# Performance work log

Measured on AMD Instinct MI355X. Metric: run time of the kernel, lower is better.

## Reference

```python
import jax, jax.numpy as jnp
import numpy as np

N_NODES = 50000
N_EDGES = 400000
NODE_F = 128
EDGE_F = 64
HID = 128
N_LAYERS = 2


def _mlp(x, w1, b1, w2, b2):
    # Linear -> ReLU -> Linear
    return jnp.maximum(x @ w1 + b1, 0.0) @ w2 + b2


def setup_inputs() -> dict:
    key = jax.random.key(0)
    ks = jax.random.split(key, 24)
    s = 0.02
    inp = {
        "node_features": jax.random.normal(ks[0], (N_NODES, NODE_F), jnp.float32),
        "edge_list": jax.random.randint(ks[1], (N_EDGES, 2), 0, N_NODES, jnp.int32),
        "edge_features": jax.random.normal(ks[2], (N_EDGES, EDGE_F), jnp.float32),
        "num_nodes": N_NODES,
        # node encoder
        "ne_w1": jax.random.normal(ks[3], (NODE_F, HID), jnp.float32) * s,
        "ne_b1": jnp.zeros((HID,), jnp.float32),
        "ne_w2": jax.random.normal(ks[4], (HID, HID), jnp.float32) * s,
        "ne_b2": jnp.zeros((HID,), jnp.float32),
        # edge encoder
        "ee_w1": jax.random.normal(ks[5], (EDGE_F, HID), jnp.float32) * s,
        "ee_b1": jnp.zeros((HID,), jnp.float32),
        "ee_w2": jax.random.normal(ks[6], (HID, HID), jnp.float32) * s,
        "ee_b2": jnp.zeros((HID,), jnp.float32),
        # message layers (stacked over num_layers)
        "ml_w1": jax.random.normal(ks[7], (N_LAYERS, 3 * HID, HID), jnp.float32) * s,
        "ml_b1": jnp.zeros((N_LAYERS, HID), jnp.float32),
        "ml_w2": jax.random.normal(ks[8], (N_LAYERS, HID, HID), jnp.float32) * s,
        "ml_b2": jnp.zeros((N_LAYERS, HID), jnp.float32),
        # aggregation
        "agg_w1": jax.random.normal(ks[9], (HID, HID), jnp.float32) * s,
        "agg_b1": jnp.zeros((HID,), jnp.float32),
        "agg_w2": jax.random.normal(ks[10], (HID, HID), jnp.float32) * s,
        "agg_b2": jnp.zeros((HID,), jnp.float32),
    }
    return inp


def reference(node_features, edge_list, edge_features, num_nodes,
              ne_w1, ne_b1, ne_w2, ne_b2,
              ee_w1, ee_b1, ee_w2, ee_b2,
              ml_w1, ml_b1, ml_w2, ml_b2,
              agg_w1, agg_b1, agg_w2, agg_b2):
    node_emb = _mlp(node_features, ne_w1, ne_b1, ne_w2, ne_b2)   # [N, H]
    edge_emb = _mlp(edge_features, ee_w1, ee_b1, ee_w2, ee_b2)   # [E, H]
    src = edge_list[:, 0]
    dst = edge_list[:, 1]
    for l in range(ml_w1.shape[0]):
        h_s = node_emb[src]                                      # [E, H] gather
        h_d = node_emb[dst]                                      # [E, H] gather
        # message src->dst and dst->src (the torch loop does both directions)
        m_fwd = _mlp(jnp.concatenate([h_s, edge_emb, h_d], axis=-1),
                     ml_w1[l], ml_b1[l], ml_w2[l], ml_b2[l])     # [E, H]
        m_bwd = _mlp(jnp.concatenate([h_d, edge_emb, h_s], axis=-1),
                     ml_w1[l], ml_b1[l], ml_w2[l], ml_b2[l])     # [E, H]
        new_node_emb = node_emb.at[dst].add(m_fwd).at[src].add(m_bwd)
        node_emb = _mlp(new_node_emb, agg_w1, agg_b1, agg_w2, agg_b2)
    return node_emb
```

## Files before the change

### kernel.cpp

```cpp
#include <hip/hip_runtime.h>

typedef float fx4 __attribute__((ext_vector_type(4)));
typedef float f32x4 __attribute__((ext_vector_type(4)));
typedef unsigned short us4v __attribute__((ext_vector_type(4)));
typedef unsigned short us8 __attribute__((ext_vector_type(8)));
typedef __bf16 bf8 __attribute__((ext_vector_type(8)));

static __device__ __forceinline__ fx4 ld4(const float* p) {
    return *reinterpret_cast<const fx4*>(p);
}
static __device__ __forceinline__ void st4(float* p, fx4 v) {
    *reinterpret_cast<fx4*>(p) = v;
}
static __device__ __forceinline__ unsigned short f2bf(float f) {
    union { float f; unsigned int i; } x; x.f = f;
    unsigned int r = x.i + 0x7FFF + ((x.i >> 16) & 1);
    return (unsigned short)(r >> 16);
}
static __device__ __forceinline__ float bf2f(unsigned int u) {
    union { unsigned int i; float f; } x; x.i = u << 16; return x.f;
}
static __device__ __forceinline__ us4v pk4(f32x4 v) {
    us4v u;
    #pragma unroll
    for (int j = 0; j < 4; ++j) u[j] = f2bf(v[j]);
    return u;
}

static __device__ __forceinline__ f32x4 mfma16(us8 a, us8 b, f32x4 c) {
    return __builtin_amdgcn_mfma_f32_16x16x32_bf16(
        __builtin_bit_cast(bf8, a), __builtin_bit_cast(bf8, b), c, 0, 0, 0);
}

template <int K1, bool AF32>
static __device__ __forceinline__ void loadA(
    const void* __restrict__ Av, int row0, int ar, int ak, int kk, int M, us8 a[2])
{
    #pragma unroll
    for (int m = 0; m < 2; ++m) {
        int row = row0 + m * 16 + ar;
        us8 t = 0;
        if (row < M) {
            if (AF32) {
                const float* ap = (const float*)Av + (size_t)row * K1 + kk * 32 + ak;
                fx4 x0 = ld4(ap), x1 = ld4(ap + 4);
                #pragma unroll
                for (int j = 0; j < 4; ++j) { t[j] = f2bf(x0[j]); t[4 + j] = f2bf(x1[j]); }
            } else {
                t = *reinterpret_cast<const us8*>(
                    (const unsigned short*)Av + (size_t)row * K1 + kk * 32 + ak);
            }
        }
        a[m] = t;
    }
}

template <int K1, bool AF32, bool BIAS, bool RELU, bool OUTF, bool OUTB, bool XMODE>
__global__ __launch_bounds__(256) void mfma_gemm(
    const void* __restrict__ Av, const unsigned short* __restrict__ Wt,
    const float* __restrict__ bias,
    float* __restrict__ outF, unsigned short* __restrict__ outB,
    const float* __restrict__ resid, const int* __restrict__ startp,
    int M, int ntiles)
{
    constexpr int KP = K1 + 8;
    __shared__ unsigned short Ws[128 * KP];
    const int tid = threadIdx.x;
    const int lane = tid & 63;
    const int wv = tid >> 6;

    constexpr int C8 = K1 / 8;
    for (int i = tid; i < 128 * C8; i += 256) {
        int r = i / C8, c = (i % C8) * 8;
        *reinterpret_cast<us8*>(&Ws[r * KP + c]) =
            *reinterpret_cast<const us8*>(&Wt[r * K1 + c]);
    }
    __syncthreads();

    const int ar = lane & 15;
    const int ak = (lane >> 4) * 8;
    const int q = lane >> 4;

    for (int tile = blockIdx.x; tile < ntiles; tile += gridDim.x) {
        const int row0 = tile * 128 + wv * 32;

        f32x4 acc[2][8];
        #pragma unroll
        for (int m = 0; m < 2; ++m)
            #pragma unroll
            for (int nt = 0; nt < 8; ++nt) acc[m][nt] = {0.f, 0.f, 0.f, 0.f};

        #pragma unroll
        for (int kk = 0; kk < K1 / 32; ++kk) {
            us8 a[2];
            loadA<K1, AF32>(Av, row0, ar, ak, kk, M, a);
            #pragma unroll
            for (int nt = 0; nt < 8; ++nt) {
                us8 b = *reinterpret_cast<const us8*>(&Ws[(nt * 16 + ar) * KP + kk * 32 + ak]);
                acc[0][nt] = mfma16(b, a[0], acc[0][nt]);
                acc[1][nt] = mfma16(b, a[1], acc[1][nt]);
            }
        }

        #pragma unroll
        for (int m = 0; m < 2; ++m) {
            int r = row0 + m * 16 + (lane & 15);
            if (r >= M) continue;
            float deg = 0.f;
            if (XMODE) deg = (float)(startp[r + 1] - startp[r]);
            #pragma unroll
            for (int nt = 0; nt < 8; ++nt) {
                int c0 = nt * 16 + q * 4;
                f32x4 o = acc[m][nt];
                if (XMODE) {
                    fx4 bb = ld4(bias + c0);
                    fx4 rr = ld4(resid + (size_t)r * 128 + c0);
                    #pragma unroll
                    for (int j = 0; j < 4; ++j) o[j] += rr[j] + deg * bb[j];
                } else if (BIAS) {
                    fx4 bb = ld4(bias + c0);
                    #pragma unroll
                    for (int j = 0; j < 4; ++j) o[j] += bb[j];
                }
                if (RELU) {
                    #pragma unroll
                    for (int j = 0; j < 4; ++j) o[j] = fmaxf(o[j], 0.f);
                }
                if (OUTF) st4(outF + (size_t)r * 128 + c0, o);
                if (OUTB) *reinterpret_cast<us4v*>(&outB[(size_t)r * 128 + c0]) = pk4(o);
            }
        }
    }
}

__global__ __launch_bounds__(256) void mfma_gemm_dual(
    const float* __restrict__ A, const unsigned short* __restrict__ Wt,
    unsigned short* __restrict__ out1, unsigned short* __restrict__ out2,
    int M, int ntiles)
{
    constexpr int KP = 136;
    __shared__ unsigned short Ws[256 * KP];
    const int tid = threadIdx.x;
    const int lane = tid & 63;
    const int wv = tid >> 6;

    for (int i = tid; i < 256 * 16; i += 256) {
        int r = i >> 4, c = (i & 15) * 8;
        *reinterpret_cast<us8*>(&Ws[r * KP + c]) =
            *reinterpret_cast<const us8*>(&Wt[r * 128 + c]);
    }
    __syncthreads();

    const int ar = lane & 15;
    const int ak = (lane >> 4) * 8;
    const int q = lane >> 4;

    for (int tile = blockIdx.x; tile < ntiles; tile += gridDim.x) {
        const int row0 = tile * 128 + wv * 32;

        f32x4 acc[2][16];
        #pragma unroll
        for (int m = 0; m < 2; ++m)
            #pragma unroll
            for (int nt = 0; nt < 16; ++nt) acc[m][nt] = {0.f, 0.f, 0.f, 0.f};

        #pragma unroll
        for (int kk = 0; kk < 4; ++kk) {
            us8 a[2];
            loadA<128, true>(A, row0, ar, ak, kk, M, a);
            #pragma unroll
            for (int nt = 0; nt < 16; ++nt) {
                us8 b = *reinterpret_cast<const us8*>(&Ws[(nt * 16 + ar) * KP + kk * 32 + ak]);
                acc[0][nt] = mfma16(b, a[0], acc[0][nt]);
                acc[1][nt] = mfma16(b, a[1], acc[1][nt]);
            }
        }

        #pragma unroll
        for (int m = 0; m < 2; ++m) {
            int r = row0 + m * 16 + (lane & 15);
            if (r >= M) continue;
            #pragma unroll
            for (int nt = 0; nt < 16; ++nt) {
                int c0 = (nt & 7) * 16 + q * 4;
                unsigned short* o = (nt < 8) ? out1 : out2;
                *reinterpret_cast<us4v*>(&o[(size_t)r * 128 + c0]) = pk4(acc[m][nt]);
            }
        }
    }
}

template <bool AF32, bool OUTF, bool OUTB>
__global__ __launch_bounds__(256) void mfma_mlp(
    const void* __restrict__ Av, const unsigned short* __restrict__ W1t,
    const float* __restrict__ b1, const unsigned short* __restrict__ W2t,
    const float* __restrict__ b2,
    float* __restrict__ outF, unsigned short* __restrict__ outB, int M)
{
    constexpr int KP = 136;
    __shared__ unsigned short Ws1[128 * KP];
    __shared__ unsigned short Ws2[128 * KP];
    const int tid = threadIdx.x;
    const int lane = tid & 63;
    const int wv = tid >> 6;
    const int row0 = blockIdx.x * 128 + wv * 32;

    for (int i = tid; i < 128 * 16; i += 256) {
        int r = i >> 4, c = (i & 15) * 8;
        *reinterpret_cast<us8*>(&Ws1[r * KP + c]) =
            *reinterpret_cast<const us8*>(&W1t[r * 128 + c]);
        *reinterpret_cast<us8*>(&Ws2[r * KP + c]) =
            *reinterpret_cast<const us8*>(&W2t[r * 128 + c]);
    }
    __syncthreads();

    const int ar = lane & 15;
    const int ak = (lane >> 4) * 8;
    const int q = lane >> 4;

    f32x4 acc[2][8];
    #pragma unroll
    for (int m = 0; m < 2; ++m)
        #pragma unroll
        for (int nt = 0; nt < 8; ++nt) acc[m][nt] = {0.f, 0.f, 0.f, 0.f};

    #pragma unroll
    for (int kk = 0; kk < 4; ++kk) {
        us8 a[2];
        loadA<128, AF32>(Av, row0, ar, ak, kk, M, a);
        #pragma unroll
        for (int nt = 0; nt < 8; ++nt) {
            us8 b = *reinterpret_cast<const us8*>(&Ws1[(nt * 16 + ar) * KP + kk * 32 + ak]);
            acc[0][nt] = mfma16(b, a[0], acc[0][nt]);
            acc[1][nt] = mfma16(b, a[1], acc[1][nt]);
        }
    }
    __syncthreads();

    #pragma unroll
    for (int m = 0; m < 2; ++m) {
        int lrow = wv * 32 + m * 16 + (lane & 15);
        #pragma unroll
        for (int nt = 0; nt < 8; ++nt) {
            int c0 = nt * 16 + q * 4;
            fx4 bb = ld4(b1 + c0);
            f32x4 o = acc[m][nt];
            #pragma unroll
            for (int j = 0; j < 4; ++j) o[j] = fmaxf(o[j] + bb[j], 0.f);
            *reinterpret_cast<us4v*>(&Ws1[lrow * KP + c0]) = pk4(o);
        }
    }
    __syncthreads();

    f32x4 acc2[2][8];
    #pragma unroll
    for (int m = 0; m < 2; ++m)
        #pragma unroll
        for (int nt = 0; nt < 8; ++nt) acc2[m][nt] = {0.f, 0.f, 0.f, 0.f};

    #pragma unroll
    for (int kk = 0; kk < 4; ++kk) {
        us8 a[2];
        #pragma unroll
        for (int m = 0; m < 2; ++m)
            a[m] = *reinterpret_cast<const us8*>(
                &Ws1[(wv * 32 + m * 16 + ar) * KP + kk * 32 + ak]);
        #pragma unroll
        for (int nt = 0; nt < 8; ++nt) {
            us8 b = *reinterpret_cast<const us8*>(&Ws2[(nt * 16 + ar) * KP + kk * 32 + ak]);
            acc2[0][nt] = mfma16(b, a[0], acc2[0][nt]);
            acc2[1][nt] = mfma16(b, a[1], acc2[1][nt]);
        }
    }

    #pragma unroll
    for (int m = 0; m < 2; ++m) {
        int r = row0 + m * 16 + (lane & 15);
        if (r >= M) continue;
        #pragma unroll
        for (int nt = 0; nt < 8; ++nt) {
            int c0 = nt * 16 + q * 4;
            fx4 bb = ld4(b2 + c0);
            f32x4 o = acc2[m][nt];
            #pragma unroll
            for (int j = 0; j < 4; ++j) o[j] += bb[j];
            if (OUTF) st4(outF + (size_t)r * 128 + c0, o);
            if (OUTB) *reinterpret_cast<us4v*>(&outB[(size_t)r * 128 + c0]) = pk4(o);
        }
    }
}

__global__ __launch_bounds__(256) void gemm128_kernel(
    const float* __restrict__ X, const float* __restrict__ W,
    float* __restrict__ Out, int M)
{
    __shared__ float Xs[64 * 132];
    const int tid = threadIdx.x;
    const int row0 = blockIdx.x * 64;

    for (int i = tid; i < 64 * 32; i += 256) {
        int r = i >> 5, c = (i & 31) * 4;
        fx4 v = {0.f, 0.f, 0.f, 0.f};
        int gr = row0 + r;
        if (gr < M) v = ld4(X + (size_t)gr * 128 + c);
        st4(&Xs[r * 132 + c], v);
    }
    __syncthreads();

    const int ty = tid >> 4, tx = tid & 15;
    fx4 acc[4][2];
    #pragma unroll
    for (int r = 0; r < 4; ++r) { acc[r][0] = 0.f; acc[r][1] = 0.f; }
    for (int k = 0; k < 128; k += 4) {
        fx4 xr[4];
        #pragma unroll
        for (int r = 0; r < 4; ++r) xr[r] = ld4(&Xs[(ty * 4 + r) * 132 + k]);
        #pragma unroll
        for (int kk = 0; kk < 4; ++kk) {
            fx4 wa = ld4(W + (size_t)(k + kk) * 128 + tx * 8);
            fx4 wb = ld4(W + (size_t)(k + kk) * 128 + tx * 8 + 4);
            #pragma unroll
            for (int r = 0; r < 4; ++r) {
                acc[r][0] += xr[r][kk] * wa;
                acc[r][1] += xr[r][kk] * wb;
            }
        }
    }
    #pragma unroll
    for (int r = 0; r < 4; ++r) {
        int gr = row0 + ty * 4 + r;
        if (gr < M) {
            st4(Out + (size_t)gr * 128 + tx * 8, acc[r][0]);
            st4(Out + (size_t)gr * 128 + tx * 8 + 4, acc[r][1]);
        }
    }
}

struct TJob { const float* src; unsigned short* dst; int K; };
struct TJobs { TJob j[16]; };

__global__ __launch_bounds__(256) void transpose_kernel(TJobs jobs) {
    TJob t = jobs.j[blockIdx.x];
    int total = 128 * t.K;
    for (int i = threadIdx.x; i < total; i += 256) {
        int n = i / t.K, k = i - n * t.K;
        t.dst[(size_t)n * t.K + k] = f2bf(t.src[(size_t)k * 128 + n]);
    }
}

__global__ __launch_bounds__(128) void bep_kernel(
    const float* __restrict__ ee_b2, const float* __restrict__ ml_w1,
    const float* __restrict__ ml_b1, float* __restrict__ bep)
{
    int l = blockIdx.x, n = threadIdx.x;
    const float* W1b = ml_w1 + (size_t)l * 384 * 128 + 128 * 128;
    float s = ml_b1[(size_t)l * 128 + n];
    for (int k = 0; k < 128; ++k) s += ee_b2[k] * W1b[(size_t)k * 128 + n];
    bep[(size_t)l * 128 + n] = s;
}

__global__ __launch_bounds__(256) void csr_hist_kernel(
    const int* __restrict__ el, int* __restrict__ cnt, int NE)
{
    int e = blockIdx.x * 256 + threadIdx.x;
    if (e < NE) {
        atomicAdd(&cnt[el[2 * (size_t)e + 1]], 1);
        atomicAdd(&cnt[el[2 * (size_t)e]], 1);
    }
}

__global__ __launch_bounds__(256) void scan_p1_kernel(
    const int* __restrict__ cnt, int* __restrict__ bsum, int NN)
{
    __shared__ int red[256];
    const int t = threadIdx.x;
    int i = blockIdx.x * 256 + t;
    red[t] = (i < NN) ? cnt[i] : 0;
    __syncthreads();
    for (int off = 128; off > 0; off >>= 1) {
        if (t < off) red[t] += red[t + off];
        __syncthreads();
    }
    if (t == 0) bsum[blockIdx.x] = red[0];
}

__global__ __launch_bounds__(256) void scan_p2_kernel(
    int* __restrict__ bsum, int* __restrict__ startp, int nb, int NN)
{
    __shared__ int part[256];
    const int t = threadIdx.x;
    int v = (t < nb) ? bsum[t] : 0;
    part[t] = v;
    __syncthreads();
    for (int off = 1; off < 256; off <<= 1) {
        int u = (t >= off) ? part[t - off] : 0;
        __syncthreads();
        part[t] += u;
        __syncthreads();
    }
    if (t < nb) bsum[t] = part[t] - v;
    if (t == 255) startp[NN] = part[255];
}

__global__ __launch_bounds__(256) void scan_p3_kernel(
    int* __restrict__ cnt, const int* __restrict__ bsum,
    int* __restrict__ startp, int NN)
{
    __shared__ int part[256];
    const int t = threadIdx.x;
    int i = blockIdx.x * 256 + t;
    int v = (i < NN) ? cnt[i] : 0;
    part[t] = v;
    __syncthreads();
    for (int off = 1; off < 256; off <<= 1) {
        int u = (t >= off) ? part[t - off] : 0;
        __syncthreads();
        part[t] += u;
        __syncthreads();
    }
    if (i < NN) {
        startp[i] = bsum[blockIdx.x] + part[t] - v;
        cnt[i] = 0;
    }
}

__global__ __launch_bounds__(256) void csr_fill_kernel(
    const int* __restrict__ el, const int* __restrict__ startp,
    int* __restrict__ cursor, int2* __restrict__ inc, int NE)
{
    int e = blockIdx.x * 256 + threadIdx.x;
    if (e < NE) {
        int s = el[2 * (size_t)e], d = el[2 * (size_t)e + 1];
        int p = startp[d] + atomicAdd(&cursor[d], 1);
        inc[p] = make_int2(s, e);
        int q = startp[s] + atomicAdd(&cursor[s], 1);
        inc[q] = make_int2(d, e);
    }
}

__global__ __launch_bounds__(256) void gather_kernel(
    const unsigned short* __restrict__ P1bf, const unsigned short* __restrict__ P3bf,
    const unsigned short* __restrict__ Ep, const int2* __restrict__ inc,
    const int* __restrict__ startp, unsigned short* __restrict__ S, int M)
{
    const int tid = threadIdx.x;
    const int lane = tid & 63;
    const int n = blockIdx.x * 4 + (tid >> 6);
    if (n >= M) return;
    const int slot = lane >> 4;
    const int c = (lane & 15) * 8;

    float p3[8], acc[8];
    us8 u3 = *reinterpret_cast<const us8*>(&P3bf[(size_t)n * 128 + c]);
    #pragma unroll
    for (int i = 0; i < 8; ++i) {
        p3[i] = bf2f((unsigned int)(unsigned short)u3[i]);
        acc[i] = 0.f;
    }

    const int j1 = startp[n + 1];
    int j = startp[n] + slot;
    int2 oe = (j < j1) ? inc[j] : make_int2(0, 0);
    while (j < j1) {
        int jn = j + 4;
        int2 oen = (jn < j1) ? inc[jn] : make_int2(0, 0);
        us8 u1 = *reinterpret_cast<const us8*>(&P1bf[(size_t)oe.x * 128 + c]);
        us8 ue = *reinterpret_cast<const us8*>(&Ep[(size_t)oe.y * 128 + c]);
        #pragma unroll
        for (int i = 0; i < 8; ++i)
            acc[i] += fmaxf(p3[i] + bf2f((unsigned int)(unsigned short)u1[i])
                                  + bf2f((unsigned int)(unsigned short)ue[i]), 0.f);
        j = jn; oe = oen;
    }

    #pragma unroll
    for (int i = 0; i < 8; ++i) {
        acc[i] += __shfl_xor(acc[i], 16, 64);
        acc[i] += __shfl_xor(acc[i], 32, 64);
    }
    if (slot == 0) {
        us8 pk;
        #pragma unroll
        for (int i = 0; i < 8; ++i) pk[i] = f2bf(acc[i]);
        *reinterpret_cast<us8*>(&S[(size_t)n * 128 + c]) = pk;
    }
}

extern "C" void kernel_launch(void* const* d_in, const int* in_sizes, int n_in,
                              void* d_out, int out_size, void* d_ws, size_t ws_size,
                              hipStream_t stream) {
    const float* node_f    = (const float*)d_in[0];
    const int*   edge_list = (const int*)d_in[1];
    const float* edge_f    = (const float*)d_in[2];
    const float* ne_w1 = (const float*)d_in[4];
    const float* ne_b1 = (const float*)d_in[5];
    const float* ne_w2 = (const float*)d_in[6];
    const float* ne_b2 = (const float*)d_in[7];
    const float* ee_w1 = (const float*)d_in[8];
    const float* ee_b1 = (const float*)d_in[9];
    const float* ee_w2 = (const float*)d_in[10];
    const float* ee_b2 = (const float*)d_in[11];
    const float* ml_w1 = (const float*)d_in[12];
    const float* ml_b1 = (const float*)d_in[13];
    const float* ml_w2 = (const float*)d_in[14];
    const float* ml_b2 = (const float*)d_in[15];
    const float* agg_w1 = (const float*)d_in[16];
    const float* agg_b1 = (const float*)d_in[17];
    const float* agg_w2 = (const float*)d_in[18];
    const float* agg_b2 = (const float*)d_in[19];

    const int NN = in_sizes[0] / 128;
    const int NE = in_sizes[1] / 2;
    const int n_layers = in_sizes[12] / (384 * 128);

    char* p = (char*)d_ws;
    auto alloc = [&](size_t bytes) -> void* {
        void* r = (void*)p;
        p += (bytes + 255) & ~(size_t)255;
        return r;
    };
    float* node_emb = (float*)alloc((size_t)NN * 128 * 4);
    unsigned short* P1bf = (unsigned short*)alloc((size_t)NN * 128 * 2);
    unsigned short* P3bf = (unsigned short*)alloc((size_t)NN * 128 * 2);
    unsigned short* bufS = (unsigned short*)alloc((size_t)NN * 128 * 2);
    unsigned short* H_edge = (unsigned short*)alloc((size_t)NE * 128 * 2);
    unsigned short* Ep = (unsigned short*)alloc((size_t)NE * 128 * 2);
    unsigned short* ne_w1t = (unsigned short*)alloc(128 * 128 * 2);
    unsigned short* ne_w2t = (unsigned short*)alloc(128 * 128 * 2);
    unsigned short* ee_w1t = (unsigned short*)alloc(128 * 64 * 2);
    unsigned short* aw1t = (unsigned short*)alloc(128 * 128 * 2);
    unsigned short* aw2t = (unsigned short*)alloc(128 * 128 * 2);
    unsigned short* W13t[2], *W2t[2], *Wept[2];
    float* Wepf[2];
    for (int l = 0; l < 2; ++l) {
        W13t[l] = (unsigned short*)alloc(256 * 128 * 2);
        W2t[l]  = (unsigned short*)alloc(128 * 128 * 2);
        Wept[l] = (unsigned short*)alloc(128 * 128 * 2);
        Wepf[l] = (float*)alloc(128 * 128 * 4);
    }
    float* bep = (float*)alloc((size_t)2 * 128 * 4);
    int* cnt = (int*)alloc((size_t)NN * 4);
    int* startp = (int*)alloc((size_t)(NN + 1) * 4);
    int* bsum = (int*)alloc(256 * 4);
    int2* inc = (int2*)alloc((size_t)2 * NE * 8);
    size_t need = (size_t)(p - (char*)d_ws);
    if (ws_size < need) return;

    dim3 blk(256);
    const int gM_N = (NN + 127) / 128;
    const int gM_E = (NE + 127) / 128;
    const int gGS_E = (gM_E < 1024) ? gM_E : 1024;
    const int gGS_N = (gM_N < 1024) ? gM_N : 1024;
    const int gE256 = (NE + 255) / 256;
    const int nbScan = (NN + 255) / 256;

    for (int l = 0; l < n_layers && l < 2; ++l) {
        const float* W1b = ml_w1 + (size_t)l * 384 * 128 + 128 * 128;
        gemm128_kernel<<<2, blk, 0, stream>>>(ee_w2, W1b, Wepf[l], 128);
    }
    {
        TJobs jobs{};
        int nj = 0;
        jobs.j[nj++] = {ne_w1, ne_w1t, 128};
        jobs.j[nj++] = {ne_w2, ne_w2t, 128};
        jobs.j[nj++] = {ee_w1, ee_w1t, 64};
        jobs.j[nj++] = {agg_w1, aw1t, 128};
        jobs.j[nj++] = {agg_w2, aw2t, 128};
        for (int l = 0; l < n_layers && l < 2; ++l) {
            jobs.j[nj++] = {ml_w1 + (size_t)l * 384 * 128, W13t[l], 128};
            jobs.j[nj++] = {ml_w1 + (size_t)l * 384 * 128 + 256 * 128, W13t[l] + 128 * 128, 128};
            jobs.j[nj++] = {ml_w2 + (size_t)l * 128 * 128, W2t[l], 128};
            jobs.j[nj++] = {Wepf[l], Wept[l], 128};
        }
        transpose_kernel<<<nj, blk, 0, stream>>>(jobs);
    }
    bep_kernel<<<n_layers, 128, 0, stream>>>(ee_b2, ml_w1, ml_b1, bep);

    mfma_mlp<true, true, false><<<gM_N, blk, 0, stream>>>(
        node_f, ne_w1t, ne_b1, ne_w2t, ne_b2, node_emb, nullptr, NN);
    mfma_gemm<64, true, true, true, false, true, false><<<gGS_E, blk, 0, stream>>>(
        edge_f, ee_w1t, ee_b1, nullptr, H_edge, nullptr, nullptr, NE, gM_E);

    hipMemsetAsync(cnt, 0, (size_t)NN * sizeof(int), stream);
    csr_hist_kernel<<<gE256, blk, 0, stream>>>(edge_list, cnt, NE);
    scan_p1_kernel<<<nbScan, blk, 0, stream>>>(cnt, bsum, NN);
    scan_p2_kernel<<<1, blk, 0, stream>>>(bsum, startp, nbScan, NN);
    scan_p3_kernel<<<nbScan, blk, 0, stream>>>(cnt, bsum, startp, NN);
    csr_fill_kernel<<<gE256, blk, 0, stream>>>(edge_list, startp, cnt, inc, NE);

    float* out = (float*)d_out;
    for (int l = 0; l < n_layers && l < 2; ++l) {
        mfma_gemm_dual<<<gM_N, blk, 0, stream>>>(node_emb, W13t[l], P1bf, P3bf, NN, gM_N);
        mfma_gemm<128, false, true, false, false, true, false><<<gGS_E, blk, 0, stream>>>(
            H_edge, Wept[l], bep + (size_t)l * 128, nullptr, Ep, nullptr, nullptr, NE, gM_E);
        gather_kernel<<<(NN + 3) / 4, blk, 0, stream>>>(
            P1bf, P3bf, Ep, inc, startp, bufS, NN);
        mfma_gemm<128, false, true, false, false, true, true><<<gGS_N, blk, 0, stream>>>(
            bufS, W2t[l], ml_b2 + (size_t)l * 128, nullptr, P1bf, node_emb, startp, NN, gM_N);
        float* dst = (l == n_layers - 1) ? out : node_emb;
        mfma_mlp<false, true, false><<<gM_N, blk, 0, stream>>>(
            P1bf, aw1t, agg_b1, aw2t, agg_b2, dst, nullptr, NN);
    }
}
```

Baseline: 623.3 us.

## Fuse edge encoder first layer with both layers' edge projections in one kernel

Adds an edge_enc2 kernel that, for each 128-edge tile, runs the first edge-encoder layer into LDS and then applies both layers' precomputed projection weights from that LDS tile. It writes Ep0 and Ep1 directly. This removes the 400K x 128 bf16 H_edge intermediate write and its two rereads, plus two per-layer edge GEMM launches. The persistent grid-stride loop in the GEMM kernels is also replaced by a plain one-tile-per-block launch. In exchange the fused kernel reads W1t and the projection weights straight from global memory rather than staging them in LDS, and keeps an extra Ep buffer live.

```diff
diff --git a/kernel.cpp b/kernel.cpp
--- a/kernel.cpp
+++ b/kernel.cpp
@@ -60,14 +60,14 @@
     const void* __restrict__ Av, const unsigned short* __restrict__ Wt,
     const float* __restrict__ bias,
     float* __restrict__ outF, unsigned short* __restrict__ outB,
-    const float* __restrict__ resid, const int* __restrict__ startp,
-    int M, int ntiles)
+    const float* __restrict__ resid, const int* __restrict__ startp, int M)
 {
     constexpr int KP = K1 + 8;
     __shared__ unsigned short Ws[128 * KP];
     const int tid = threadIdx.x;
     const int lane = tid & 63;
     const int wv = tid >> 6;
+    const int row0 = blockIdx.x * 128 + wv * 32;
 
     constexpr int C8 = K1 / 8;
     for (int i = tid; i < 128 * C8; i += 256) {
@@ -81,111 +81,50 @@
     const int ak = (lane >> 4) * 8;
     const int q = lane >> 4;
 
-    for (int tile = blockIdx.x; tile < ntiles; tile += gridDim.x) {
-        const int row0 = tile * 128 + wv * 32;
-
-        f32x4 acc[2][8];
-        #pragma unroll
-        for (int m = 0; m < 2; ++m)
-            #pragma unroll
-            for (int nt = 0; nt < 8; ++nt) acc[m][nt] = {0.f, 0.f, 0.f, 0.f};
-
-        #pragma unroll
-        for (int kk = 0; kk < K1 / 32; ++kk) {
-            us8 a[2];
-            loadA<K1, AF32>(Av, row0, ar, ak, kk, M, a);
-            #pragma unroll
-            for (int nt = 0; nt < 8; ++nt) {
-                us8 b = *reinterpret_cast<const us8*>(&Ws[(nt * 16 + ar) * KP + kk * 32 + ak]);
-                acc[0][nt] = mfma16(b, a[0], acc[0][nt]);
-                acc[1][nt] = mfma16(b, a[1], acc[1][nt]);
+    f32x4 acc[2][8];
+    #pragma unroll
+    for (int m = 0; m < 2; ++m)
+        #pragma unroll
+        for (int nt = 0; nt < 8; ++nt) acc[m][nt] = {0.f, 0.f, 0.f, 0.f};
+
+    #pragma unroll
+    for (int kk = 0; kk < K1 / 32; ++kk) {
+        us8 a[2];
+        loadA<K1, AF32>(Av, row0, ar, ak, kk, M, a);
+        #pragma unroll
+        for (int nt = 0; nt < 8; ++nt) {
+            us8 b = *reinterpret_cast<const us8*>(&Ws[(nt * 16 + ar) * KP + kk * 32 + ak]);
+            acc[0][nt] = mfma16(b, a[0], acc[0][nt]);
+            acc[1][nt] = mfma16(b, a[1], acc[1][nt]);
+        }
+    }
+
+    #pragma unroll
+    for (int m = 0; m < 2; ++m) {
+        int r = row0 + m * 16 + (lane & 15);
+        if (r >= M) continue;
+        float deg = 0.f;
+        if (XMODE) deg = (float)(startp[r + 1] - startp[r]);
+        #pragma unroll
+        for (int nt = 0; nt < 8; ++nt) {
+            int c0 = nt * 16 + q * 4;
+            f32x4 o = acc[m][nt];
+            if (XMODE) {
+                fx4 bb = ld4(bias + c0);
+                fx4 rr = ld4(resid + (size_t)r * 128 + c0);
+                #pragma unroll
+                for (int j = 0; j < 4; ++j) o[j] += rr[j] + deg * bb[j];
+            } else if (BIAS) {
+                fx4 bb = ld4(bias + c0);
+                #pragma unroll
+                for (int j = 0; j < 4; ++j) o[j] += bb[j];
             }
-        }
-
-        #pragma unroll
-        for (int m = 0; m < 2; ++m) {
-            int r = row0 + m * 16 + (lane & 15);
-            if (r >= M) continue;
-            float deg = 0.f;
-            if (XMODE) deg = (float)(startp[r + 1] - startp[r]);
-            #pragma unroll
-            for (int nt = 0; nt < 8; ++nt) {
-                int c0 = nt * 16 + q * 4;
-                f32x4 o = acc[m][nt];
-                if (XMODE) {
-                    fx4 bb = ld4(bias + c0);
-                    fx4 rr = ld4(resid + (size_t)r * 128 + c0);
-                    #pragma unroll
-                    for (int j = 0; j < 4; ++j) o[j] += rr[j] + deg * bb[j];
-                } else if (BIAS) {
-                    fx4 bb = ld4(bias + c0);
-                    #pragma unroll
-                    for (int j = 0; j < 4; ++j) o[j] += bb[j];
-                }
-                if (RELU) {
-                    #pragma unroll
-                    for (int j = 0; j < 4; ++j) o[j] = fmaxf(o[j], 0.f);
-                }
-                if (OUTF) st4(outF + (size_t)r * 128 + c0, o);
-                if (OUTB) *reinterpret_cast<us4v*>(&outB[(size_t)r * 128 + c0]) = pk4(o);
+            if (RELU) {
+                #pragma unroll
+                for (int j = 0; j < 4; ++j) o[j] = fmaxf(o[j], 0.f);
             }
-        }
-    }
-}
-
-__global__ __launch_bounds__(256) void mfma_gemm_dual(
-    const float* __restrict__ A, const unsigned short* __restrict__ Wt,
-    unsigned short* __restrict__ out1, unsigned short* __restrict__ out2,
-    int M, int ntiles)
-{
-    constexpr int KP = 136;
-    __shared__ unsigned short Ws[256 * KP];
-    const int tid = threadIdx.x;
-    const int lane = tid & 63;
-    const int wv = tid >> 6;
-
-    for (int i = tid; i < 256 * 16; i += 256) {
-        int r = i >> 4, c = (i & 15) * 8;
-        *reinterpret_cast<us8*>(&Ws[r * KP + c]) =
-            *reinterpret_cast<const us8*>(&Wt[r * 128 + c]);
-    }
-    __syncthreads();
-
-    const int ar = lane & 15;
-    const int ak = (lane >> 4) * 8;
-    const int q = lane >> 4;
-
-    for (int tile = blockIdx.x; tile < ntiles; tile += gridDim.x) {
-        const int row0 = tile * 128 + wv * 32;
-
-        f32x4 acc[2][16];
-        #pragma unroll
-        for (int m = 0; m < 2; ++m)
-            #pragma unroll
-            for (int nt = 0; nt < 16; ++nt) acc[m][nt] = {0.f, 0.f, 0.f, 0.f};
-
-        #pragma unroll
-        for (int kk = 0; kk < 4; ++kk) {
-            us8 a[2];
-            loadA<128, true>(A, row0, ar, ak, kk, M, a);
-            #pragma unroll
-            for (int nt = 0; nt < 16; ++nt) {
-                us8 b = *reinterpret_cast<const us8*>(&Ws[(nt * 16 + ar) * KP + kk * 32 + ak]);
-                acc[0][nt] = mfma16(b, a[0], acc[0][nt]);
-                acc[1][nt] = mfma16(b, a[1], acc[1][nt]);
-            }
-        }
-
-        #pragma unroll
-        for (int m = 0; m < 2; ++m) {
-            int r = row0 + m * 16 + (lane & 15);
-            if (r >= M) continue;
-            #pragma unroll
-            for (int nt = 0; nt < 16; ++nt) {
-                int c0 = (nt & 7) * 16 + q * 4;
-                unsigned short* o = (nt < 8) ? out1 : out2;
-                *reinterpret_cast<us4v*>(&o[(size_t)r * 128 + c0]) = pk4(acc[m][nt]);
-            }
+            if (OUTF) st4(outF + (size_t)r * 128 + c0, o);
+            if (OUTB) *reinterpret_cast<us4v*>(&outB[(size_t)r * 128 + c0]) = pk4(o);
         }
     }
 }
@@ -286,6 +225,172 @@
             for (int j = 0; j < 4; ++j) o[j] += bb[j];
             if (OUTF) st4(outF + (size_t)r * 128 + c0, o);
             if (OUTB) *reinterpret_cast<us4v*>(&outB[(size_t)r * 128 + c0]) = pk4(o);
+        }
+    }
+}
+
+__global__ __launch_bounds__(256) void mfma_gemm_dual(
+    const float* __restrict__ A, const unsigned short* __restrict__ Wt,
+    unsigned short* __restrict__ out1, unsigned short* __restrict__ out2, int M)
+{
+    constexpr int KP = 136;
+    __shared__ unsigned short Ws[256 * KP];
+    const int tid = threadIdx.x;
+    const int lane = tid & 63;
+    const int wv = tid >> 6;
+    const int row0 = blockIdx.x * 128 + wv * 32;
+
+    for (int i = tid; i < 256 * 16; i += 256) {
+        int r = i >> 4, c = (i & 15) * 8;
+        *reinterpret_cast<us8*>(&Ws[r * KP + c]) =
+            *reinterpret_cast<const us8*>(&Wt[r * 128 + c]);
+    }
+    __syncthreads();
+
+    const int ar = lane & 15;
+    const int ak = (lane >> 4) * 8;
+    const int q = lane >> 4;
+
+    f32x4 acc[2][16];
+    #pragma unroll
+    for (int m = 0; m < 2; ++m)
+        #pragma unroll
+        for (int nt = 0; nt < 16; ++nt) acc[m][nt] = {0.f, 0.f, 0.f, 0.f};
+
+    #pragma unroll
+    for (int kk = 0; kk < 4; ++kk) {
+        us8 a[2];
+        loadA<128, true>(A, row0, ar, ak, kk, M, a);
+        #pragma unroll
+        for (int nt = 0; nt < 16; ++nt) {
+            us8 b = *reinterpret_cast<const us8*>(&Ws[(nt * 16 + ar) * KP + kk * 32 + ak]);
+            acc[0][nt] = mfma16(b, a[0], acc[0][nt]);
+            acc[1][nt] = mfma16(b, a[1], acc[1][nt]);
+        }
+    }
+
+    #pragma unroll
+    for (int m = 0; m < 2; ++m) {
+        int r = row0 + m * 16 + (lane & 15);
+        if (r >= M) continue;
+        #pragma unroll
+        for (int nt = 0; nt < 16; ++nt) {
+            int c0 = (nt & 7) * 16 + q * 4;
+            unsigned short* o = (nt < 8) ? out1 : out2;
+            *reinterpret_cast<us4v*>(&o[(size_t)r * 128 + c0]) = pk4(acc[m][nt]);
+        }
+    }
+}
+
+__global__ __launch_bounds__(256) void edge_enc2(
+    const float* __restrict__ edge_f,
+    const unsigned short* __restrict__ W1t,
+    const float* __restrict__ b1,
+    const unsigned short* __restrict__ Wep0t,
+    const unsigned short* __restrict__ Wep1t,
+    const float* __restrict__ bep,
+    unsigned short* __restrict__ Ep0, unsigned short* __restrict__ Ep1,
+    int nl, int M)
+{
+    constexpr int KP = 136;
+    __shared__ unsigned short Hs[128 * KP];
+    const int tid = threadIdx.x;
+    const int lane = tid & 63;
+    const int wv = tid >> 6;
+    const int row0 = blockIdx.x * 128 + wv * 32;
+
+    const int ar = lane & 15;
+    const int q = lane >> 4;
+    const int ak = q * 8;
+
+    {
+        const int lr = lane >> 4;
+        const int lc = (lane & 15) * 4;
+        #pragma unroll
+        for (int j = 0; j < 8; ++j) {
+            int row = row0 + j * 4 + lr;
+            fx4 v = {0.f, 0.f, 0.f, 0.f};
+            if (row < M) v = ld4(edge_f + (size_t)row * 64 + lc);
+            *reinterpret_cast<us4v*>(&Hs[(wv * 32 + j * 4 + lr) * KP + lc]) = pk4(v);
+        }
+    }
+
+    f32x4 acc[2][8];
+    #pragma unroll
+    for (int m = 0; m < 2; ++m)
+        #pragma unroll
+        for (int nt = 0; nt < 8; ++nt) acc[m][nt] = {0.f, 0.f, 0.f, 0.f};
+
+    #pragma unroll
+    for (int kk = 0; kk < 2; ++kk) {
+        us8 a[2];
+        #pragma unroll
+        for (int m = 0; m < 2; ++m)
+            a[m] = *reinterpret_cast<const us8*>(
+                &Hs[(wv * 32 + m * 16 + ar) * KP + kk * 32 + ak]);
+        #pragma unroll
+        for (int nt = 0; nt < 8; ++nt) {
+            us8 b = *reinterpret_cast<const us8*>(
+                &W1t[(size_t)(nt * 16 + ar) * 64 + kk * 32 + ak]);
+            acc[0][nt] = mfma16(b, a[0], acc[0][nt]);
+            acc[1][nt] = mfma16(b, a[1], acc[1][nt]);
+        }
+    }
+
+    #pragma unroll
+    for (int m = 0; m < 2; ++m) {
+        int lrow = wv * 32 + m * 16 + (lane & 15);
+        #pragma unroll
+        for (int nt = 0; nt < 8; ++nt) {
+            int c0 = nt * 16 + q * 4;
+            fx4 bb = ld4(b1 + c0);
+            f32x4 o = acc[m][nt];
+            #pragma unroll
+            for (int j = 0; j < 4; ++j) o[j] = fmaxf(o[j] + bb[j], 0.f);
+            *reinterpret_cast<us4v*>(&Hs[lrow * KP + c0]) = pk4(o);
+        }
+    }
+
+    for (int l = 0; l < nl; ++l) {
+        const unsigned short* Wt = (l == 0) ? Wep0t : Wep1t;
+        unsigned short* Out = (l == 0) ? Ep0 : Ep1;
+        const float* bl = bep + (size_t)l * 128;
+
+        f32x4 acc2[2][8];
+        #pragma unroll
+        for (int m = 0; m < 2; ++m)
+            #pragma unroll
+            for (int nt = 0; nt < 8; ++nt) acc2[m][nt] = {0.f, 0.f, 0.f, 0.f};
+
+        #pragma unroll
+        for (int kk = 0; kk < 4; ++kk) {
+            us8 a[2];
+            #pragma unroll
+            for (int m = 0; m < 2; ++m)
+                a[m] = *reinterpret_cast<const us8*>(
+                    &Hs[(wv * 32 + m * 16 + ar) * KP + kk * 32 + ak]);
+            #pragma unroll
+            for (int nt = 0; nt < 8; ++nt) {
+                us8 b = *reinterpret_cast<const us8*>(
+                    &Wt[(size_t)(nt * 16 + ar) * 128 + kk * 32 + ak]);
+                acc2[0][nt] = mfma16(b, a[0], acc2[0][nt]);
+                acc2[1][nt] = mfma16(b, a[1], acc2[1][nt]);
+            }
+        }
+
+        #pragma unroll
+        for (int m = 0; m < 2; ++m) {
+            int r = row0 + m * 16 + (lane & 15);
+            if (r >= M) continue;
+            #pragma unroll
+            for (int nt = 0; nt < 8; ++nt) {
+                int c0 = nt * 16 + q * 4;
+                fx4 bb = ld4(bl + c0);
+                f32x4 o = acc2[m][nt];
+                #pragma unroll
+                for (int j = 0; j < 4; ++j) o[j] += bb[j];
+                *reinterpret_cast<us4v*>(&Out[(size_t)r * 128 + c0]) = pk4(o);
+            }
         }
     }
 }
@@ -523,8 +628,8 @@
     unsigned short* P1bf = (unsigned short*)alloc((size_t)NN * 128 * 2);
     unsigned short* P3bf = (unsigned short*)alloc((size_t)NN * 128 * 2);
     unsigned short* bufS = (unsigned short*)alloc((size_t)NN * 128 * 2);
-    unsigned short* H_edge = (unsigned short*)alloc((size_t)NE * 128 * 2);
-    unsigned short* Ep = (unsigned short*)alloc((size_t)NE * 128 * 2);
+    unsigned short* Ep0 = (unsigned short*)alloc((size_t)NE * 128 * 2);
+    unsigned short* Ep1 = (unsigned short*)alloc((size_t)NE * 128 * 2);
     unsigned short* ne_w1t = (unsigned short*)alloc(128 * 128 * 2);
     unsigned short* ne_w2t = (unsigned short*)alloc(128 * 128 * 2);
     unsigned short* ee_w1t = (unsigned short*)alloc(128 * 64 * 2);
@@ -549,8 +654,6 @@
     dim3 blk(256);
     const int gM_N = (NN + 127) / 128;
     const int gM_E = (NE + 127) / 128;
-    const int gGS_E = (gM_E < 1024) ? gM_E : 1024;
-    const int gGS_N = (gM_N < 1024) ? gM_N : 1024;
     const int gE256 = (NE + 255) / 256;
     const int nbScan = (NN + 255) / 256;
 
@@ -578,8 +681,9 @@
 
     mfma_mlp<true, true, false><<<gM_N, blk, 0, stream>>>(
         node_f, ne_w1t, ne_b1, ne_w2t, ne_b2, node_emb, nullptr, NN);
-    mfma_gemm<64, true, true, true, false, true, false><<<gGS_E, blk, 0, stream>>>(
-        edge_f, ee_w1t, ee_b1, nullptr, H_edge, nullptr, nullptr, NE, gM_E);
+    edge_enc2<<<gM_E, blk, 0, stream>>>(
+        edge_f, ee_w1t, ee_b1, Wept[0], Wept[(n_layers > 1) ? 1 : 0], bep,
+        Ep0, Ep1, (n_layers > 1) ? 2 : 1, NE);
 
     hipMemsetAsync(cnt, 0, (size_t)NN * sizeof(int), stream);
     csr_hist_kernel<<<gE256, blk, 0, stream>>>(edge_list, cnt, NE);
@@ -590,13 +694,11 @@
 
     float* out = (float*)d_out;
     for (int l = 0; l < n_layers && l < 2; ++l) {
-        mfma_gemm_dual<<<gM_N, blk, 0, stream>>>(node_emb, W13t[l], P1bf, P3bf, NN, gM_N);
-        mfma_gemm<128, false, true, false, false, true, false><<<gGS_E, blk, 0, stream>>>(
-            H_edge, Wept[l], bep + (size_t)l * 128, nullptr, Ep, nullptr, nullptr, NE, gM_E);
+        mfma_gemm_dual<<<gM_N, blk, 0, stream>>>(node_emb, W13t[l], P1bf, P3bf, NN);
         gather_kernel<<<(NN + 3) / 4, blk, 0, stream>>>(
-            P1bf, P3bf, Ep, inc, startp, bufS, NN);
-        mfma_gemm<128, false, true, false, false, true, true><<<gGS_N, blk, 0, stream>>>(
-            bufS, W2t[l], ml_b2 + (size_t)l * 128, nullptr, P1bf, node_emb, startp, NN, gM_N);
+            P1bf, P3bf, (l == 0) ? Ep0 : Ep1, inc, startp, bufS, NN);
+        mfma_gemm<128, false, true, false, false, true, true><<<gM_N, blk, 0, stream>>>(
+            bufS, W2t[l], ml_b2 + (size_t)l * 128, nullptr, P1bf, node_emb, startp, NN);
         float* dst = (l == n_layers - 1) ? out : node_emb;
         mfma_mlp<false, true, false><<<gM_N, blk, 0, stream>>>(
             P1bf, aw1t, agg_b1, aw2t, agg_b2, dst, nullptr, NN);
```

Measured after the change: 652.8 us. 1.05x slower.
